# Performance work log

Measured on AMD Instinct MI355X. Metric: run time of the kernel, lower is better.

Reference implementation:

```python
import jax, jax.numpy as jnp
import numpy as np

B, T, Dx, H, K = 32, 4096, 128, 128, 10


def setup_inputs() -> dict:
    key = jax.random.key(0)
    ks = jax.random.split(key, 11)
    s = 1.0 / np.sqrt(H)  # PyTorch GRU init range

    def p(k, shape):
        return jax.random.uniform(k, shape, jnp.float32, -s, s)

    return {
        "x": jax.random.normal(ks[0], (B, T, Dx), jnp.float32),
        # forward-direction GRU params (gate order: r, z, n as in PyTorch)
        "W_ih_f": p(ks[1], (3 * H, Dx)),
        "W_hh_f": p(ks[2], (3 * H, H)),
        "b_ih_f": p(ks[3], (3 * H,)),
        "b_hh_f": p(ks[4], (3 * H,)),
        # backward-direction GRU params
        "W_ih_b": p(ks[5], (3 * H, Dx)),
        "W_hh_b": p(ks[6], (3 * H, H)),
        "b_ih_b": p(ks[7], (3 * H,)),
        "b_hh_b": p(ks[8], (3 * H,)),
        # final linear classifier
        "W_fc": p(ks[9], (K, 2 * H)),
        "b_fc": p(ks[10], (K,)),
    }


def _gru_scan(x, Wih, Whh, bih, bhh, reverse):
    """Single-direction GRU over time. x: [B,T,Dx] -> [B,T,H]."""
    # Precompute all input projections at once: [T, B, 3H]
    xp = jnp.einsum('btd,gd->tbg', x, Wih) + bih
    Whh_T = Whh.T
    Hd = Whh.shape[1]

    def cell(h, xt):
        hp = h @ Whh_T + bhh            # [B, 3H]
        xr, xz, xn = jnp.split(xt, 3, axis=-1)
        hr, hz, hn = jnp.split(hp, 3, axis=-1)
        r = jax.nn.sigmoid(xr + hr)
        z = jax.nn.sigmoid(xz + hz)
        n = jnp.tanh(xn + r * hn)
        h_new = (1.0 - z) * n + z * h
        return h_new, h_new

    h0 = jnp.zeros((x.shape[0], Hd), x.dtype)
    _, hs = jax.lax.scan(cell, h0, xp, reverse=reverse)  # [T, B, H]
    return jnp.transpose(hs, (1, 0, 2))


def reference(x, W_ih_f, W_hh_f, b_ih_f, b_hh_f,
              W_ih_b, W_hh_b, b_ih_b, b_hh_b, W_fc, b_fc):
    hf = _gru_scan(x, W_ih_f, W_hh_f, b_ih_f, b_hh_f, reverse=False)
    hb = _gru_scan(x, W_ih_b, W_hh_b, b_ih_b, b_hh_b, reverse=True)
    h = jnp.concatenate([hf, hb], axis=-1)  # [B, T, 2H]
    return h @ W_fc.T + b_fc                # [B, T, K]
```

## Files before the change

kernel.cpp:

```cpp
#include <hip/hip_runtime.h>
#include <cstdint>
#include <cstddef>

#define T_LEN   4096
#define B_SZ    32
#define H_DIM   128
#define DX      128
#define K_CLS   10
#define CHUNK   32
#define NCHUNKS (T_LEN / CHUNK)
#define WMAT    (3 * H_DIM * DX)
#define XA_LD   136
#define XP_LD   520
#define HI_LD   136

typedef _Float16 half2v  __attribute__((ext_vector_type(2)));
typedef _Float16 half8   __attribute__((ext_vector_type(8)));
typedef float    floatx4 __attribute__((ext_vector_type(4)));

__device__ __forceinline__ float dot2f(unsigned int w, unsigned int h, float acc) {
  return __builtin_amdgcn_fdot2(__builtin_bit_cast(half2v, w),
                                __builtin_bit_cast(half2v, h), acc, false);
}

__device__ __forceinline__ unsigned int packh2(float a, float b) {
  half2v h;
  h.x = (_Float16)a;
  h.y = (_Float16)b;
  return __builtin_bit_cast(unsigned int, h);
}

__device__ __forceinline__ float dpp_xor1_add(float x) {
  int xi = __builtin_bit_cast(int, x);
  int yi = __builtin_amdgcn_update_dpp(xi, xi, 0xB1, 0xF, 0xF, false);
  return x + __builtin_bit_cast(float, yi);
}

__device__ __forceinline__ float sigm(float x) {
  return __builtin_amdgcn_rcpf(1.f + __expf(-x));
}

__device__ __forceinline__ float tanhfast(float x) {
  x = fmaxf(x, -15.f);
  float t = __expf(-2.f * x);
  return (1.f - t) * __builtin_amdgcn_rcpf(1.f + t);
}

__device__ __forceinline__ void bar_lgkm() {
  asm volatile("s_waitcnt lgkmcnt(0)\n\ts_barrier" ::: "memory");
}

__global__ void __launch_bounds__(256) init_out_kernel(float* __restrict__ out,
                                                       const float* __restrict__ bfc) {
  int i = blockIdx.x * 256 + threadIdx.x;
  if (i < B_SZ * T_LEN * K_CLS) out[i] = bfc[i % K_CLS];
}

__global__ void __launch_bounds__(256) cvt_wih_kernel(const float* __restrict__ a,
                                                      const float* __restrict__ b,
                                                      _Float16* __restrict__ o) {
  int i = blockIdx.x * 256 + threadIdx.x;
  if (i < WMAT) {
    o[i]        = (_Float16)a[i];
    o[WMAT + i] = (_Float16)b[i];
  }
}

__global__ void __launch_bounds__(256, 1)
gru_scan_kernel(const float* __restrict__ x,
                const float* __restrict__ Whh_f, const float* __restrict__ bih_f,
                const float* __restrict__ bhh_f,
                const float* __restrict__ Whh_b, const float* __restrict__ bih_b,
                const float* __restrict__ bhh_b,
                const _Float16* __restrict__ w16,
                const float* __restrict__ Wfc, float* __restrict__ out) {
  const int tid = threadIdx.x;
  const int bid = blockIdx.x;
  const int dir = bid >> 5;
  const int b   = bid & (B_SZ - 1);

  const float* Whh = dir ? Whh_b : Whh_f;
  const float* bih = dir ? bih_b : bih_f;
  const float* bhh = dir ? bhh_b : bhh_f;
  const _Float16* Wih16 = w16 + (size_t)dir * WMAT;

  const int lane = tid & 63;
  const int wv   = tid >> 6;
  const int col  = lane & 15;
  const int quad = lane >> 4;

  const int j = tid >> 1;
  const int q = tid & 1;

  __shared__ __align__(16) _Float16 xAf[CHUNK * XA_LD];
  __shared__ __align__(16) _Float16 xpL[CHUNK * XP_LD];
  __shared__ __align__(16) _Float16 histf[CHUNK * HI_LD];

  unsigned int whr[32], whz[32], whn[32];
  {
    const float* Wr = Whh + (size_t)j * H_DIM + q * 64;
    const float* Wz = Whh + (size_t)(H_DIM + j) * H_DIM + q * 64;
    const float* Wn = Whh + (size_t)(2 * H_DIM + j) * H_DIM + q * 64;
#pragma unroll
    for (int i = 0; i < 32; ++i) {
      whr[i] = packh2(Wr[2 * i], Wr[2 * i + 1]);
      whz[i] = packh2(Wz[2 * i], Wz[2 * i + 1]);
      whn[i] = packh2(Wn[2 * i], Wn[2 * i + 1]);
    }
  }
  const float cbr  = bih[j] + bhh[j];
  const float cbz  = bih[H_DIM + j] + bhh[H_DIM + j];
  const float bin_ = bih[2 * H_DIM + j];
  const float bhn  = bhh[2 * H_DIM + j];

  half8 fcfrag[4];
#pragma unroll
  for (int ks = 0; ks < 4; ++ks) {
    half8 v;
#pragma unroll
    for (int e = 0; e < 8; ++e) {
      int cc = ks * 32 + quad * 8 + e;
      v[e] = (col < K_CLS) ? (_Float16)Wfc[(size_t)col * (2 * H_DIM) + dir * H_DIM + cc]
                           : (_Float16)0.f;
    }
    fcfrag[ks] = v;
  }

  if (tid < 64) ((unsigned int*)&histf[31 * HI_LD])[tid] = 0u;

  const int prow  = tid >> 3;
  const int cbase = (tid & 7) * 16;
  float4 px0, px1, px2, px3;
  {
    int t0 = dir ? (T_LEN - 1 - prow) : prow;
    const float* xp = x + ((size_t)b * T_LEN + t0) * DX + cbase;
    px0 = *(const float4*)xp;       px1 = *(const float4*)(xp + 4);
    px2 = *(const float4*)(xp + 8); px3 = *(const float4*)(xp + 12);
  }

  float hold = 0.f;
  __syncthreads();

  for (int ck = 0; ck < NCHUNKS; ++ck) {
    {
      half8 lo, hi;
      lo[0] = (_Float16)px0.x; lo[1] = (_Float16)px0.y; lo[2] = (_Float16)px0.z; lo[3] = (_Float16)px0.w;
      lo[4] = (_Float16)px1.x; lo[5] = (_Float16)px1.y; lo[6] = (_Float16)px1.z; lo[7] = (_Float16)px1.w;
      hi[0] = (_Float16)px2.x; hi[1] = (_Float16)px2.y; hi[2] = (_Float16)px2.z; hi[3] = (_Float16)px2.w;
      hi[4] = (_Float16)px3.x; hi[5] = (_Float16)px3.y; hi[6] = (_Float16)px3.z; hi[7] = (_Float16)px3.w;
      *(half8*)&xAf[prow * XA_LD + cbase] = lo;
      *(half8*)&xAf[prow * XA_LD + cbase + 8] = hi;
    }
    bar_lgkm();

    {
#pragma unroll
      for (int nt = 0; nt < 6; ++nt) {
        const int gg = (wv * 6 + nt) * 16 + col;
        const _Float16* wsrc = Wih16 + (size_t)gg * DX + quad * 8;
        half8 bf0 = *(const half8*)(wsrc);
        half8 bf1 = *(const half8*)(wsrc + 32);
        half8 bf2 = *(const half8*)(wsrc + 64);
        half8 bf3 = *(const half8*)(wsrc + 96);
        floatx4 a0 = (floatx4){0.f, 0.f, 0.f, 0.f};
        floatx4 a1 = (floatx4){0.f, 0.f, 0.f, 0.f};
#pragma unroll
        for (int mt = 0; mt < 2; ++mt) {
          const _Float16* ab = &xAf[(mt * 16 + col) * XA_LD + quad * 8];
          floatx4& ac = mt ? a1 : a0;
          ac = __builtin_amdgcn_mfma_f32_16x16x32_f16(*(const half8*)(ab),      bf0, ac, 0, 0, 0);
          ac = __builtin_amdgcn_mfma_f32_16x16x32_f16(*(const half8*)(ab + 32), bf1, ac, 0, 0, 0);
          ac = __builtin_amdgcn_mfma_f32_16x16x32_f16(*(const half8*)(ab + 64), bf2, ac, 0, 0, 0);
          ac = __builtin_amdgcn_mfma_f32_16x16x32_f16(*(const half8*)(ab + 96), bf3, ac, 0, 0, 0);
        }
        const int jj = (gg & 127) * 4 + (gg >> 7);
#pragma unroll
        for (int i = 0; i < 4; ++i) {
          xpL[(quad * 4 + i) * XP_LD + jj]      = (_Float16)a0[i];
          xpL[(16 + quad * 4 + i) * XP_LD + jj] = (_Float16)a1[i];
        }
      }
      if (ck + 1 < NCHUNKS) {
        int t = (ck + 1) * CHUNK + prow;
        int t0 = dir ? (T_LEN - 1 - t) : t;
        const float* xp = x + ((size_t)b * T_LEN + t0) * DX + cbase;
        px0 = *(const float4*)xp;       px1 = *(const float4*)(xp + 4);
        px2 = *(const float4*)(xp + 8); px3 = *(const float4*)(xp + 12);
      }
    }
    bar_lgkm();

#pragma unroll 8
    for (int s = 0; s < CHUNK; ++s) {
      const int pr = (s + 31) & 31;
      const uint4* hb = (const uint4*)&histf[pr * HI_LD + q * 64];
      uint4 H0 = hb[0], H1 = hb[1], H2 = hb[2], H3 = hb[3];
      uint4 H4 = hb[4], H5 = hb[5], H6 = hb[6], H7 = hb[7];
      uint2 xv = *(const uint2*)&xpL[s * XP_LD + j * 4];

      unsigned int hh[32];
      hh[0]  = H0.x; hh[1]  = H0.y; hh[2]  = H0.z; hh[3]  = H0.w;
      hh[4]  = H1.x; hh[5]  = H1.y; hh[6]  = H1.z; hh[7]  = H1.w;
      hh[8]  = H2.x; hh[9]  = H2.y; hh[10] = H2.z; hh[11] = H2.w;
      hh[12] = H3.x; hh[13] = H3.y; hh[14] = H3.z; hh[15] = H3.w;
      hh[16] = H4.x; hh[17] = H4.y; hh[18] = H4.z; hh[19] = H4.w;
      hh[20] = H5.x; hh[21] = H5.y; hh[22] = H5.z; hh[23] = H5.w;
      hh[24] = H6.x; hh[25] = H6.y; hh[26] = H6.z; hh[27] = H6.w;
      hh[28] = H7.x; hh[29] = H7.y; hh[30] = H7.z; hh[31] = H7.w;

      float ar0 = 0.f, ar1 = 0.f, az0 = 0.f, az1 = 0.f, an0 = 0.f, an1 = 0.f;
#pragma unroll
      for (int i = 0; i < 16; ++i) {
        ar0 = dot2f(whr[2 * i],     hh[2 * i],     ar0);
        ar1 = dot2f(whr[2 * i + 1], hh[2 * i + 1], ar1);
        az0 = dot2f(whz[2 * i],     hh[2 * i],     az0);
        az1 = dot2f(whz[2 * i + 1], hh[2 * i + 1], az1);
        an0 = dot2f(whn[2 * i],     hh[2 * i],     an0);
        an1 = dot2f(whn[2 * i + 1], hh[2 * i + 1], an1);
      }
      float ar = dpp_xor1_add(ar0 + ar1);
      float az = dpp_xor1_add(az0 + az1);
      float an = dpp_xor1_add(an0 + an1);

      half2v x01 = __builtin_bit_cast(half2v, xv.x);
      half2v x23 = __builtin_bit_cast(half2v, xv.y);
      float rr = sigm((float)x01.x + cbr + ar);
      float zz = sigm((float)x01.y + cbz + az);
      float nn = tanhfast((float)x23.x + bin_ + rr * (an + bhn));
      hold = nn + zz * (hold - nn);

      if (q == 0) histf[s * HI_LD + j] = (_Float16)hold;
      bar_lgkm();
    }

    if (wv < 2) {
      floatx4 facc = (floatx4){0.f, 0.f, 0.f, 0.f};
#pragma unroll
      for (int ks = 0; ks < 4; ++ks) {
        half8 af = *(const half8*)&histf[(wv * 16 + col) * HI_LD + ks * 32 + quad * 8];
        facc = __builtin_amdgcn_mfma_f32_16x16x32_f16(af, fcfrag[ks], facc, 0, 0, 0);
      }
      if (col < K_CLS) {
#pragma unroll
        for (int i = 0; i < 4; ++i) {
          int s  = wv * 16 + quad * 4 + i;
          int t  = ck * CHUNK + s;
          int tt = dir ? (T_LEN - 1 - t) : t;
          atomicAdd(out + ((size_t)b * T_LEN + tt) * K_CLS + col, facc[i]);
        }
      }
    }
  }
}

extern "C" void kernel_launch(void* const* d_in, const int* in_sizes, int n_in,
                              void* d_out, int out_size, void* d_ws, size_t ws_size,
                              hipStream_t stream) {
  (void)in_sizes; (void)n_in; (void)ws_size; (void)out_size;
  const float* x     = (const float*)d_in[0];
  const float* Wih_f = (const float*)d_in[1];
  const float* Whh_f = (const float*)d_in[2];
  const float* bih_f = (const float*)d_in[3];
  const float* bhh_f = (const float*)d_in[4];
  const float* Wih_b = (const float*)d_in[5];
  const float* Whh_b = (const float*)d_in[6];
  const float* bih_b = (const float*)d_in[7];
  const float* bhh_b = (const float*)d_in[8];
  const float* Wfc   = (const float*)d_in[9];
  const float* bfc   = (const float*)d_in[10];
  float* out = (float*)d_out;

  _Float16* w16 = (_Float16*)d_ws;

  const int n_out = B_SZ * T_LEN * K_CLS;
  init_out_kernel<<<(n_out + 255) / 256, 256, 0, stream>>>(out, bfc);
  cvt_wih_kernel<<<(WMAT + 255) / 256, 256, 0, stream>>>(Wih_f, Wih_b, w16);
  gru_scan_kernel<<<B_SZ * 2, 256, 0, stream>>>(x, Whh_f, bih_f, bhh_f,
                                                Whh_b, bih_b, bhh_b,
                                                w16, Wfc, out);
}
```

Measured before the change: 2.119 ms.

## Share hidden-state chunks across lanes with DPP row rotates instead of LDS reads

```diff
diff --git a/kernel.cpp b/kernel.cpp
--- a/kernel.cpp
+++ b/kernel.cpp
@@ -30,6 +30,21 @@
   return __builtin_bit_cast(unsigned int, h);
 }
 
+template <int N>
+__device__ __forceinline__ unsigned int ror16(unsigned int v) {
+  return (unsigned int)__builtin_amdgcn_update_dpp((int)v, (int)v, 0x120 + N, 0xF, 0xF, false);
+}
+
+template <int N>
+__device__ __forceinline__ uint4 ror16x4(uint4 v) {
+  uint4 r;
+  r.x = ror16<N>(v.x);
+  r.y = ror16<N>(v.y);
+  r.z = ror16<N>(v.z);
+  r.w = ror16<N>(v.w);
+  return r;
+}
+
 __device__ __forceinline__ float dpp_xor1_add(float x) {
   int xi = __builtin_bit_cast(int, x);
   int yi = __builtin_amdgcn_update_dpp(xi, xi, 0xB1, 0xF, 0xF, false);
@@ -44,10 +59,6 @@
   x = fmaxf(x, -15.f);
   float t = __expf(-2.f * x);
   return (1.f - t) * __builtin_amdgcn_rcpf(1.f + t);
-}
-
-__device__ __forceinline__ void bar_lgkm() {
-  asm volatile("s_waitcnt lgkmcnt(0)\n\ts_barrier" ::: "memory");
 }
 
 __global__ void __launch_bounds__(256) init_out_kernel(float* __restrict__ out,
@@ -91,6 +102,8 @@
 
   const int j = tid >> 1;
   const int q = tid & 1;
+  const int k8 = (lane >> 1) & 7;
+  const int cch = k8 + q * 8;
 
   __shared__ __align__(16) _Float16 xAf[CHUNK * XA_LD];
   __shared__ __align__(16) _Float16 xpL[CHUNK * XP_LD];
@@ -98,14 +111,18 @@
 
   unsigned int whr[32], whz[32], whn[32];
   {
-    const float* Wr = Whh + (size_t)j * H_DIM + q * 64;
-    const float* Wz = Whh + (size_t)(H_DIM + j) * H_DIM + q * 64;
-    const float* Wn = Whh + (size_t)(2 * H_DIM + j) * H_DIM + q * 64;
-#pragma unroll
-    for (int i = 0; i < 32; ++i) {
-      whr[i] = packh2(Wr[2 * i], Wr[2 * i + 1]);
-      whz[i] = packh2(Wz[2 * i], Wz[2 * i + 1]);
-      whn[i] = packh2(Wn[2 * i], Wn[2 * i + 1]);
+    const float* Wr = Whh + (size_t)j * H_DIM;
+    const float* Wz = Whh + (size_t)(H_DIM + j) * H_DIM;
+    const float* Wn = Whh + (size_t)(2 * H_DIM + j) * H_DIM;
+#pragma unroll
+    for (int i = 0; i < 8; ++i) {
+      const int cb = q * 64 + (((k8 - i) & 7) * 8);
+#pragma unroll
+      for (int m = 0; m < 4; ++m) {
+        whr[i * 4 + m] = packh2(Wr[cb + 2 * m], Wr[cb + 2 * m + 1]);
+        whz[i * 4 + m] = packh2(Wz[cb + 2 * m], Wz[cb + 2 * m + 1]);
+        whn[i * 4 + m] = packh2(Wn[cb + 2 * m], Wn[cb + 2 * m + 1]);
+      }
     }
   }
   const float cbr  = bih[j] + bhh[j];
@@ -151,7 +168,7 @@
       *(half8*)&xAf[prow * XA_LD + cbase] = lo;
       *(half8*)&xAf[prow * XA_LD + cbase + 8] = hi;
     }
-    bar_lgkm();
+    __syncthreads();
 
     {
 #pragma unroll
@@ -188,49 +205,74 @@
         px2 = *(const float4*)(xp + 8); px3 = *(const float4*)(xp + 12);
       }
     }
-    bar_lgkm();
-
-#pragma unroll 8
-    for (int s = 0; s < CHUNK; ++s) {
-      const int pr = (s + 31) & 31;
-      const uint4* hb = (const uint4*)&histf[pr * HI_LD + q * 64];
-      uint4 H0 = hb[0], H1 = hb[1], H2 = hb[2], H3 = hb[3];
-      uint4 H4 = hb[4], H5 = hb[5], H6 = hb[6], H7 = hb[7];
-      uint2 xv = *(const uint2*)&xpL[s * XP_LD + j * 4];
-
-      unsigned int hh[32];
-      hh[0]  = H0.x; hh[1]  = H0.y; hh[2]  = H0.z; hh[3]  = H0.w;
-      hh[4]  = H1.x; hh[5]  = H1.y; hh[6]  = H1.z; hh[7]  = H1.w;
-      hh[8]  = H2.x; hh[9]  = H2.y; hh[10] = H2.z; hh[11] = H2.w;
-      hh[12] = H3.x; hh[13] = H3.y; hh[14] = H3.z; hh[15] = H3.w;
-      hh[16] = H4.x; hh[17] = H4.y; hh[18] = H4.z; hh[19] = H4.w;
-      hh[20] = H5.x; hh[21] = H5.y; hh[22] = H5.z; hh[23] = H5.w;
-      hh[24] = H6.x; hh[25] = H6.y; hh[26] = H6.z; hh[27] = H6.w;
-      hh[28] = H7.x; hh[29] = H7.y; hh[30] = H7.z; hh[31] = H7.w;
-
-      float ar0 = 0.f, ar1 = 0.f, az0 = 0.f, az1 = 0.f, an0 = 0.f, an1 = 0.f;
-#pragma unroll
-      for (int i = 0; i < 16; ++i) {
-        ar0 = dot2f(whr[2 * i],     hh[2 * i],     ar0);
-        ar1 = dot2f(whr[2 * i + 1], hh[2 * i + 1], ar1);
-        az0 = dot2f(whz[2 * i],     hh[2 * i],     az0);
-        az1 = dot2f(whz[2 * i + 1], hh[2 * i + 1], az1);
-        an0 = dot2f(whn[2 * i],     hh[2 * i],     an0);
-        an1 = dot2f(whn[2 * i + 1], hh[2 * i + 1], an1);
-      }
-      float ar = dpp_xor1_add(ar0 + ar1);
-      float az = dpp_xor1_add(az0 + az1);
-      float an = dpp_xor1_add(an0 + an1);
-
-      half2v x01 = __builtin_bit_cast(half2v, xv.x);
-      half2v x23 = __builtin_bit_cast(half2v, xv.y);
-      float rr = sigm((float)x01.x + cbr + ar);
-      float zz = sigm((float)x01.y + cbz + az);
-      float nn = tanhfast((float)x23.x + bin_ + rr * (an + bhn));
-      hold = nn + zz * (hold - nn);
-
-      if (q == 0) histf[s * HI_LD + j] = (_Float16)hold;
-      bar_lgkm();
+    __syncthreads();
+
+#pragma unroll 1
+    for (int g = 0; g < 4; ++g) {
+      uint2 xg[8];
+#pragma unroll
+      for (int u = 0; u < 8; ++u)
+        xg[u] = *(const uint2*)&xpL[(g * 8 + u) * XP_LD + j * 4];
+
+#pragma unroll
+      for (int u = 0; u < 8; ++u) {
+        const int s  = g * 8 + u;
+        const int pr = (s + 31) & 31;
+        uint4 h0 = *(const uint4*)&histf[pr * HI_LD + cch * 8];
+        uint4 hr1 = ror16<2>(h0.x)  ? (uint4){0,0,0,0} : (uint4){0,0,0,0};
+        (void)hr1;
+        uint4 hs[8];
+        hs[0] = h0;
+        hs[1] = ror16x4<2>(h0);
+        hs[2] = ror16x4<4>(h0);
+        hs[3] = ror16x4<6>(h0);
+        hs[4] = ror16x4<8>(h0);
+        hs[5] = ror16x4<10>(h0);
+        hs[6] = ror16x4<12>(h0);
+        hs[7] = ror16x4<14>(h0);
+
+        float ar0 = 0.f, ar1 = 0.f, az0 = 0.f, az1 = 0.f, an0 = 0.f, an1 = 0.f;
+#pragma unroll
+        for (int i = 0; i < 8; i += 2) {
+          ar0 = dot2f(whr[i * 4 + 0], hs[i].x, ar0);
+          ar0 = dot2f(whr[i * 4 + 1], hs[i].y, ar0);
+          ar0 = dot2f(whr[i * 4 + 2], hs[i].z, ar0);
+          ar0 = dot2f(whr[i * 4 + 3], hs[i].w, ar0);
+          ar1 = dot2f(whr[i * 4 + 4], hs[i + 1].x, ar1);
+          ar1 = dot2f(whr[i * 4 + 5], hs[i + 1].y, ar1);
+          ar1 = dot2f(whr[i * 4 + 6], hs[i + 1].z, ar1);
+          ar1 = dot2f(whr[i * 4 + 7], hs[i + 1].w, ar1);
+          az0 = dot2f(whz[i * 4 + 0], hs[i].x, az0);
+          az0 = dot2f(whz[i * 4 + 1], hs[i].y, az0);
+          az0 = dot2f(whz[i * 4 + 2], hs[i].z, az0);
+          az0 = dot2f(whz[i * 4 + 3], hs[i].w, az0);
+          az1 = dot2f(whz[i * 4 + 4], hs[i + 1].x, az1);
+          az1 = dot2f(whz[i * 4 + 5], hs[i + 1].y, az1);
+          az1 = dot2f(whz[i * 4 + 6], hs[i + 1].z, az1);
+          az1 = dot2f(whz[i * 4 + 7], hs[i + 1].w, az1);
+          an0 = dot2f(whn[i * 4 + 0], hs[i].x, an0);
+          an0 = dot2f(whn[i * 4 + 1], hs[i].y, an0);
+          an0 = dot2f(whn[i * 4 + 2], hs[i].z, an0);
+          an0 = dot2f(whn[i * 4 + 3], hs[i].w, an0);
+          an1 = dot2f(whn[i * 4 + 4], hs[i + 1].x, an1);
+          an1 = dot2f(whn[i * 4 + 5], hs[i + 1].y, an1);
+          an1 = dot2f(whn[i * 4 + 6], hs[i + 1].z, an1);
+          an1 = dot2f(whn[i * 4 + 7], hs[i + 1].w, an1);
+        }
+        float ar = dpp_xor1_add(ar0 + ar1);
+        float az = dpp_xor1_add(az0 + az1);
+        float an = dpp_xor1_add(an0 + an1);
+
+        half2v x01 = __builtin_bit_cast(half2v, xg[u].x);
+        half2v x23 = __builtin_bit_cast(half2v, xg[u].y);
+        float rr = sigm((float)x01.x + cbr + ar);
+        float zz = sigm((float)x01.y + cbz + az);
+        float nn = tanhfast((float)x23.x + bin_ + rr * (an + bhn));
+        hold = nn + zz * (hold - nn);
+
+        if (q == 0) histf[s * HI_LD + j] = (_Float16)hold;
+        __syncthreads();
+      }
     }
 
     if (wv < 2) {
```

Result: no change. 2.082 ms (-1.8%).
